# Performance work log

Measured on AMD Instinct MI355X. Metric: run time of the kernel, lower is better.

The kernel has to match this reference:

```python
import jax, jax.numpy as jnp
import numpy as np

N = 10000      # n_nodes
T = 8          # input_horizon
P = 2          # prediction_horizon (zeros appended; pred_hor=1 default)
F_IN = 64      # n_features
F_OUT = 64     # n_out_features
H = 128        # h_size
B = 2          # batch
E = 160000     # n_edges
MLPW = 4


def setup_inputs() -> dict:
    key = jax.random.key(0)
    ks = jax.random.split(key, 12)
    s = jnp.float32(0.05)
    return dict(
        x_in=jax.random.normal(ks[0], (B, T, N, F_IN), jnp.float32),
        edge_index=jax.random.randint(ks[1], (2, E), 0, N, jnp.int32),
        edge_weight=jax.random.uniform(ks[2], (E,), jnp.float32),
        gcn_w=jax.random.normal(ks[3], (F_OUT, F_IN), jnp.float32) * s,
        gcn_b=jnp.zeros((F_OUT,), jnp.float32),
        w_ih=jax.random.normal(ks[4], (H, F_OUT), jnp.float32) * s,
        w_hh=jax.random.normal(ks[5], (H, H), jnp.float32) * s,
        b_ih=jnp.zeros((H,), jnp.float32),
        b_hh=jnp.zeros((H,), jnp.float32),
        mlp_w1=jax.random.normal(ks[6], (H * MLPW, H), jnp.float32) * s,
        mlp_b1=jnp.zeros((H * MLPW,), jnp.float32),
        mlp_w2=jax.random.normal(ks[7], (H * MLPW, H * MLPW), jnp.float32) * s,
        mlp_b2=jnp.zeros((H * MLPW,), jnp.float32),
        mlp_w3=jax.random.normal(ks[8], (F_OUT, H * MLPW), jnp.float32) * s,
        mlp_b3=jnp.zeros((F_OUT,), jnp.float32),
    )


def reference(x_in, edge_index, edge_weight, gcn_w, gcn_b,
              w_ih, w_hh, b_ih, b_hh,
              mlp_w1, mlp_b1, mlp_w2, mlp_b2, mlp_w3, mlp_b3):
    Bb = x_in.shape[0]
    x = x_in.reshape(-1, N, F_IN)          # [G, N, F_in], G = B*T
    G = x.shape[0]

    # --- python id-remap (unique -> dense ids); identity when all node ids appear ---
    uv = jnp.unique(edge_index, size=N)
    ei = jnp.searchsorted(uv, edge_index)
    row, col = ei[0], ei[1]

    # --- GCNConv (gcn_norm with add_self_loops=True, fill 1.0) ---
    loop = jnp.arange(N, dtype=row.dtype)
    row_f = jnp.concatenate([row, loop])
    col_f = jnp.concatenate([col, loop])
    ew_f = jnp.concatenate([edge_weight, jnp.ones((N,), edge_weight.dtype)])
    deg = jnp.zeros((N,), edge_weight.dtype).at[col_f].add(ew_f)
    dinv = jnp.where(deg > 0, jax.lax.rsqrt(deg), 0.0)
    norm = dinv[row_f] * ew_f * dinv[col_f]          # [E+N]

    xl = x @ gcn_w.T                                 # [G, N, F_out]
    agg = jnp.zeros((G, N, F_OUT), xl.dtype).at[:, col_f].add(
        xl[:, row_f] * norm[None, :, None])          # scatter-add over targets
    gc = agg + gcn_b                                 # [G, N, F_out]

    # raw row-major view, exactly as torch .view((B*N, T, F_out))
    seq = gc.reshape(Bb * N, T, F_OUT)

    # --- single-layer tanh RNN, batch_first ---
    h0 = jnp.zeros((Bb * N, H), seq.dtype)

    def step(h, xt):
        h = jnp.tanh(xt @ w_ih.T + b_ih + h @ w_hh.T + b_hh)
        return h, h

    _, outs = jax.lax.scan(step, h0, seq.transpose(1, 0, 2))  # [T, B*N, H]
    rnn_out = outs.transpose(1, 0, 2)                          # [B*N, T, H]

    # --- MLP head applied per time step (vectorized) ---
    y = jax.nn.relu(rnn_out @ mlp_w1.T + mlp_b1)
    y = jax.nn.relu(y @ mlp_w2.T + mlp_b2)
    y = y @ mlp_w3.T + mlp_b3                                  # [B*N, T, F_out]

    # prediction slots stay zero (pred_hor=1 default)
    full = jnp.concatenate([y, jnp.zeros((Bb * N, P, F_OUT), y.dtype)], axis=1)
    return full.reshape(Bb, T + P, N, F_OUT)
```

## Files before the change

kernel.cpp:

```cpp
#include <hip/hip_runtime.h>
#include <hip/hip_bf16.h>

#define N_NODES 10000
#define E_EDGES 160000

typedef __attribute__((ext_vector_type(8))) short bf16x8;
typedef __attribute__((ext_vector_type(4))) float f32x4;

__device__ __forceinline__ unsigned short f2b(float f) {
    unsigned int u = __float_as_uint(f);
    u = (u + 0x7fffu + ((u >> 16) & 1u)) >> 16;
    return (unsigned short)u;
}

__device__ __forceinline__ float b2f(unsigned short u) {
    return __uint_as_float(((unsigned int)u) << 16);
}

__device__ __forceinline__ float tanh_fast(float x) {
    float ax = fabsf(x);
    float e = __expf(-2.f * ax);
    float r = (1.f - e) / (1.f + e);
    return copysignf(r, x);
}

__global__ void init_kernel(float* deg, int* cnt) {
    int i = blockIdx.x * 256 + threadIdx.x;
    if (i < N_NODES) { deg[i] = 1.0f; cnt[i] = 0; }
}

__global__ void deg_add_kernel(const int* __restrict__ ei, const float* __restrict__ ew,
                               float* deg, int* cnt) {
    int e = blockIdx.x * 256 + threadIdx.x;
    if (e < E_EDGES) {
        int c = ei[E_EDGES + e];
        atomicAdd(&deg[c], ew[e]);
        atomicAdd(&cnt[c], 1);
    }
}

__global__ void dinv_kernel(const float* __restrict__ deg, float* dinv) {
    int i = blockIdx.x * 256 + threadIdx.x;
    if (i < N_NODES) { float d = deg[i]; dinv[i] = d > 0.f ? rsqrtf(d) : 0.f; }
}

__global__ void scan_kernel(const int* __restrict__ cnt, int* offs, int* cursor) {
    __shared__ int tsum[1024];
    int t = threadIdx.x;
    int base = t * 10;
    int loc[10];
    int s = 0;
    #pragma unroll
    for (int j = 0; j < 10; ++j) {
        int i = base + j;
        int v = (i < N_NODES) ? cnt[i] : 0;
        loc[j] = s; s += v;
    }
    tsum[t] = s;
    __syncthreads();
    for (int d = 1; d < 1024; d <<= 1) {
        int v = (t >= d) ? tsum[t - d] : 0;
        __syncthreads();
        tsum[t] += v;
        __syncthreads();
    }
    int pre = tsum[t] - s;
    #pragma unroll
    for (int j = 0; j < 10; ++j) {
        int i = base + j;
        if (i < N_NODES) { offs[i] = pre + loc[j]; cursor[i] = pre + loc[j]; }
    }
    if (t == 1023) offs[N_NODES] = tsum[1023];
}

__global__ void fill_kernel(const int* __restrict__ ei, const float* __restrict__ ew,
                            const float* __restrict__ dinv, int* cursor,
                            int* erow, float* enorm) {
    int e = blockIdx.x * 256 + threadIdx.x;
    if (e < E_EDGES) {
        int r = ei[e], c = ei[E_EDGES + e];
        float nm = dinv[r] * ew[e] * dinv[c];
        int pos = atomicAdd(&cursor[c], 1);
        erow[pos] = r; enorm[pos] = nm;
    }
}

template<int KS, int K>
__global__ void wconv_kernel(const float* __restrict__ w, unsigned short* __restrict__ o) {
    int idx = blockIdx.x * 256 + threadIdx.x;
    int lane = idx & 63, frag = idx >> 6;
    int nf = frag / KS, ks = frag % KS;
    const float* src = w + (nf * 16 + (lane & 15)) * K + ks * 32 + (lane >> 4) * 8;
    unsigned short* dst = o + frag * 512 + lane * 8;
    float4 v0 = *(const float4*)src;
    float4 v1 = *(const float4*)(src + 4);
    ushort4 h0; h0.x = f2b(v0.x); h0.y = f2b(v0.y); h0.z = f2b(v0.z); h0.w = f2b(v0.w);
    ushort4 h1; h1.x = f2b(v1.x); h1.y = f2b(v1.y); h1.z = f2b(v1.z); h1.w = f2b(v1.w);
    *(ushort4*)dst = h0;
    *(ushort4*)(dst + 4) = h1;
}

__global__ __launch_bounds__(256) void aggregate_kernel(
        const unsigned short* __restrict__ xlt, const int* __restrict__ erow,
        const float* __restrict__ enorm, const int* __restrict__ offs,
        const float* __restrict__ dinv, const float* __restrict__ gcn_b,
        unsigned short* __restrict__ gc) {
    int gwid = (blockIdx.x * 256 + threadIdx.x) >> 6;
    int c = gwid >> 1;
    int gh = (gwid & 1) * 8;
    int lane = threadIdx.x & 63;
    if (c >= N_NODES) return;
    float acc[8];
    float d = dinv[c];
    float wself = d * d;
    const unsigned short* xr = xlt + (long)c * 1024 + gh * 64;
    #pragma unroll
    for (int g = 0; g < 8; ++g) acc[g] = b2f(xr[g * 64 + lane]) * wself;
    int e0 = offs[c], e1 = offs[c + 1];
    for (int e = e0; e < e1; ++e) {
        int r = erow[e];
        float nm = enorm[e];
        const unsigned short* xs = xlt + (long)r * 1024 + gh * 64;
        #pragma unroll
        for (int g = 0; g < 8; ++g) acc[g] += b2f(xs[g * 64 + lane]) * nm;
    }
    float bb = gcn_b[lane];
    #pragma unroll
    for (int g = 0; g < 8; ++g)
        gc[(long)(gh + g) * 640000 + (long)c * 64 + lane] = f2b(acc[g] + bb);
}

template<int NTOT, int BN, int KTOT, bool AF32, int EPI, bool RELU>
__global__ __launch_bounds__(256) void gemm_kernel(
        const void* __restrict__ Aptr, const float* __restrict__ Wp,
        const float* __restrict__ bias0, const float* __restrict__ bias1,
        void* __restrict__ outp) {
    constexpr int WN = BN / 2;
    constexpr int FN = WN / 16;
    __shared__ __align__(16) unsigned short As[128 * 72];
    __shared__ __align__(16) unsigned short Bs[BN * 72];
    const int tid = threadIdx.x;
    const int lane = tid & 63;
    const int wid = tid >> 6;
    const int wm = wid >> 1, wn = wid & 1;
    const long m0 = (long)blockIdx.x * 128;
    const int n0 = blockIdx.y * BN;

    f32x4 acc[4][FN];
    #pragma unroll
    for (int a = 0; a < 4; ++a)
        #pragma unroll
        for (int b = 0; b < FN; ++b)
            acc[a][b] = (f32x4){0.f, 0.f, 0.f, 0.f};

    for (int kt = 0; kt < KTOT / 64; ++kt) {
        if (AF32) {
            const float* Ag = (const float*)Aptr;
            #pragma unroll
            for (int p = 0; p < 8; ++p) {
                int idx = p * 256 + tid;
                int r = idx >> 4, c4 = idx & 15;
                float4 v = *(const float4*)(Ag + (m0 + r) * KTOT + kt * 64 + c4 * 4);
                ushort4 h; h.x = f2b(v.x); h.y = f2b(v.y); h.z = f2b(v.z); h.w = f2b(v.w);
                *(ushort4*)&As[r * 72 + c4 * 4] = h;
            }
        } else {
            const unsigned short* Ag = (const unsigned short*)Aptr;
            #pragma unroll
            for (int p = 0; p < 4; ++p) {
                int idx = p * 256 + tid;
                int r = idx >> 3, c8 = idx & 7;
                *(int4*)&As[r * 72 + c8 * 8] = *(const int4*)(Ag + (m0 + r) * KTOT + kt * 64 + c8 * 8);
            }
        }
        #pragma unroll
        for (int p = 0; p < BN / 16; ++p) {
            int idx = p * 256 + tid;
            int r = idx >> 4, c4 = idx & 15;
            float4 v = *(const float4*)(Wp + (long)(n0 + r) * KTOT + kt * 64 + c4 * 4);
            ushort4 h; h.x = f2b(v.x); h.y = f2b(v.y); h.z = f2b(v.z); h.w = f2b(v.w);
            *(ushort4*)&Bs[r * 72 + c4 * 4] = h;
        }
        __syncthreads();
        #pragma unroll
        for (int ks = 0; ks < 2; ++ks) {
            bf16x8 a[4], b[FN];
            #pragma unroll
            for (int fm = 0; fm < 4; ++fm)
                a[fm] = *(const bf16x8*)&As[(wm * 64 + fm * 16 + (lane & 15)) * 72 + ks * 32 + (lane >> 4) * 8];
            #pragma unroll
            for (int fn = 0; fn < FN; ++fn)
                b[fn] = *(const bf16x8*)&Bs[(wn * WN + fn * 16 + (lane & 15)) * 72 + ks * 32 + (lane >> 4) * 8];
            #pragma unroll
            for (int fm = 0; fm < 4; ++fm)
                #pragma unroll
                for (int fn = 0; fn < FN; ++fn)
                    acc[fm][fn] = __builtin_amdgcn_mfma_f32_16x16x32_bf16(a[fm], b[fn], acc[fm][fn], 0, 0, 0);
        }
        __syncthreads();
    }

    #pragma unroll
    for (int fm = 0; fm < 4; ++fm) {
        #pragma unroll
        for (int fn = 0; fn < FN; ++fn) {
            const int colg = n0 + wn * WN + fn * 16 + (lane & 15);
            float bv = 0.f;
            if (bias0) bv += bias0[colg];
            if (bias1) bv += bias1[colg];
            #pragma unroll
            for (int r = 0; r < 4; ++r) {
                int row = (int)m0 + wm * 64 + fm * 16 + (lane >> 4) * 4 + r;
                float v = acc[fm][fn][r] + bv;
                if (RELU) v = fmaxf(v, 0.f);
                if (EPI == 0) {
                    ((unsigned short*)outp)[(long)(row % N_NODES) * 1024 + (long)(row / N_NODES) * 64 + colg] = f2b(v);
                } else {
                    ((unsigned short*)outp)[(long)row * NTOT + colg] = f2b(v);
                }
            }
        }
    }
}

__global__ __launch_bounds__(256) void rnn_kernel(const unsigned short* __restrict__ xih,
                                                  const float* __restrict__ whh,
                                                  unsigned short* __restrict__ rout) {
    __shared__ __align__(16) unsigned short hs[80 * 128];
    __shared__ __align__(16) unsigned short ws[128 * 128];
    const int tid = threadIdx.x, lane = tid & 63, wid = tid >> 6;
    const long i0 = (long)blockIdx.x * 80;

    #pragma unroll
    for (int p = 0; p < 16; ++p) {
        int idx = p * 256 + tid;
        int n = idx >> 5, k4 = (idx & 31) * 4;
        float4 v = *(const float4*)(whh + n * 128 + k4);
        ushort4 h; h.x = f2b(v.x); h.y = f2b(v.y); h.z = f2b(v.z); h.w = f2b(v.w);
        int byte = (n * 256 + k4 * 2) ^ ((n & 7) << 4);
        *(ushort4*)((char*)ws + byte) = h;
    }
    int4 z = make_int4(0, 0, 0, 0);
    #pragma unroll
    for (int p = 0; p < 5; ++p) ((int4*)hs)[p * 256 + tid] = z;
    __syncthreads();

    unsigned short x2[2][5][2][4];
    #pragma unroll
    for (int fm = 0; fm < 5; ++fm)
        #pragma unroll
        for (int fn = 0; fn < 2; ++fn) {
            int col = wid * 32 + fn * 16 + (lane & 15);
            const unsigned short* src = xih + ((i0 + fm * 16 + (lane >> 4) * 4) * 8 + 0) * 128 + col;
            #pragma unroll
            for (int r = 0; r < 4; ++r) x2[0][fm][fn][r] = src[(long)r * 1024];
        }

    f32x4 acc[5][2];
    #pragma unroll
    for (int t = 0; t < 8; ++t) {
        const int cb = t & 1;
        #pragma unroll
        for (int fm = 0; fm < 5; ++fm)
            #pragma unroll
            for (int fn = 0; fn < 2; ++fn)
                #pragma unroll
                for (int r = 0; r < 4; ++r)
                    acc[fm][fn][r] = b2f(x2[cb][fm][fn][r]);
        if (t < 7) {
            #pragma unroll
            for (int fm = 0; fm < 5; ++fm)
                #pragma unroll
                for (int fn = 0; fn < 2; ++fn) {
                    int col = wid * 32 + fn * 16 + (lane & 15);
                    const unsigned short* src = xih + ((i0 + fm * 16 + (lane >> 4) * 4) * 8 + (t + 1)) * 128 + col;
                    #pragma unroll
                    for (int r = 0; r < 4; ++r) x2[cb ^ 1][fm][fn][r] = src[(long)r * 1024];
                }
        }
        #pragma unroll
        for (int ks = 0; ks < 4; ++ks) {
            bf16x8 a[5], b[2];
            #pragma unroll
            for (int fm = 0; fm < 5; ++fm) {
                int row = fm * 16 + (lane & 15);
                int byte = (row * 256 + ks * 64 + (lane >> 4) * 16) ^ ((row & 7) << 4);
                a[fm] = *(const bf16x8*)((const char*)hs + byte);
            }
            #pragma unroll
            for (int fn = 0; fn < 2; ++fn) {
                int rowb = wid * 32 + fn * 16 + (lane & 15);
                int byte = (rowb * 256 + ks * 64 + (lane >> 4) * 16) ^ ((rowb & 7) << 4);
                b[fn] = *(const bf16x8*)((const char*)ws + byte);
            }
            #pragma unroll
            for (int fm = 0; fm < 5; ++fm)
                #pragma unroll
                for (int fn = 0; fn < 2; ++fn)
                    acc[fm][fn] = __builtin_amdgcn_mfma_f32_16x16x32_bf16(a[fm], b[fn], acc[fm][fn], 0, 0, 0);
        }
        __syncthreads();
        #pragma unroll
        for (int fm = 0; fm < 5; ++fm)
            #pragma unroll
            for (int fn = 0; fn < 2; ++fn) {
                int col = wid * 32 + fn * 16 + (lane & 15);
                #pragma unroll
                for (int r = 0; r < 4; ++r) {
                    int row = fm * 16 + (lane >> 4) * 4 + r;
                    float v = tanh_fast(acc[fm][fn][r]);
                    unsigned short hb = f2b(v);
                    int byte = (row * 256 + col * 2) ^ ((row & 7) << 4);
                    *(unsigned short*)((char*)hs + byte) = hb;
                    rout[((i0 + row) * 8 + t) * 128 + col] = hb;
                }
            }
        __syncthreads();
    }
}

__global__ __launch_bounds__(512) void mlp_kernel(
        const unsigned short* __restrict__ A,
        const unsigned short* __restrict__ w1f, const float* __restrict__ b1,
        const unsigned short* __restrict__ w2f, const float* __restrict__ b2,
        const unsigned short* __restrict__ w3f, const float* __restrict__ b3,
        float* __restrict__ out) {
    __shared__ __align__(16) char smem[147456];
    char* As  = smem;
    char* y1s = smem + 16384;
    char* y2s = smem + 81920;
    float* red = (float*)smem;

    const int tid = threadIdx.x, lane = tid & 63, w = tid >> 6;
    const long r0 = (long)blockIdx.x * 64;

    #pragma unroll
    for (int p = 0; p < 2; ++p) {
        int idx = p * 512 + tid;
        int row = idx >> 4, c16 = idx & 15;
        int4 v = *(const int4*)(A + (r0 + row) * 128 + c16 * 8);
        int byte = (row * 256 + c16 * 16) ^ ((row & 7) << 4);
        *(int4*)(As + byte) = v;
    }
    __syncthreads();

    f32x4 acc[4][4];

    #pragma unroll
    for (int fm = 0; fm < 4; ++fm)
        #pragma unroll
        for (int fn = 0; fn < 4; ++fn) acc[fm][fn] = (f32x4){0.f, 0.f, 0.f, 0.f};
    #pragma unroll
    for (int ks = 0; ks < 4; ++ks) {
        bf16x8 a[4], b[4];
        #pragma unroll
        for (int fm = 0; fm < 4; ++fm) {
            int row = fm * 16 + (lane & 15);
            a[fm] = *(const bf16x8*)(As + ((row * 256 + ks * 64 + (lane >> 4) * 16) ^ ((row & 7) << 4)));
        }
        #pragma unroll
        for (int fn = 0; fn < 4; ++fn)
            b[fn] = *(const bf16x8*)(w1f + (long)((w * 4 + fn) * 4 + ks) * 512 + lane * 8);
        #pragma unroll
        for (int fm = 0; fm < 4; ++fm)
            #pragma unroll
            for (int fn = 0; fn < 4; ++fn)
                acc[fm][fn] = __builtin_amdgcn_mfma_f32_16x16x32_bf16(a[fm], b[fn], acc[fm][fn], 0, 0, 0);
    }
    #pragma unroll
    for (int fn = 0; fn < 4; ++fn) {
        int colg = w * 64 + fn * 16 + (lane & 15);
        float bv = b1[colg];
        #pragma unroll
        for (int fm = 0; fm < 4; ++fm)
            #pragma unroll
            for (int r = 0; r < 4; ++r) {
                int row = fm * 16 + (lane >> 4) * 4 + r;
                float v = fmaxf(acc[fm][fn][r] + bv, 0.f);
                int byte = (row * 1024 + colg * 2) ^ ((row & 7) << 4);
                *(unsigned short*)(y1s + byte) = f2b(v);
            }
    }
    __syncthreads();

    #pragma unroll
    for (int fm = 0; fm < 4; ++fm)
        #pragma unroll
        for (int fn = 0; fn < 4; ++fn) acc[fm][fn] = (f32x4){0.f, 0.f, 0.f, 0.f};
    #pragma unroll
    for (int ks = 0; ks < 16; ++ks) {
        bf16x8 a[4], b[4];
        #pragma unroll
        for (int fm = 0; fm < 4; ++fm) {
            int row = fm * 16 + (lane & 15);
            a[fm] = *(const bf16x8*)(y1s + ((row * 1024 + ks * 64 + (lane >> 4) * 16) ^ ((row & 7) << 4)));
        }
        #pragma unroll
        for (int fn = 0; fn < 4; ++fn)
            b[fn] = *(const bf16x8*)(w2f + (long)((w * 4 + fn) * 16 + ks) * 512 + lane * 8);
        #pragma unroll
        for (int fm = 0; fm < 4; ++fm)
            #pragma unroll
            for (int fn = 0; fn < 4; ++fn)
                acc[fm][fn] = __builtin_amdgcn_mfma_f32_16x16x32_bf16(a[fm], b[fn], acc[fm][fn], 0, 0, 0);
    }
    #pragma unroll
    for (int fn = 0; fn < 4; ++fn) {
        int colg = w * 64 + fn * 16 + (lane & 15);
        float bv = b2[colg];
        #pragma unroll
        for (int fm = 0; fm < 4; ++fm)
            #pragma unroll
            for (int r = 0; r < 4; ++r) {
                int row = fm * 16 + (lane >> 4) * 4 + r;
                float v = fmaxf(acc[fm][fn][r] + bv, 0.f);
                int byte = (row * 1024 + colg * 2) ^ ((row & 7) << 4);
                *(unsigned short*)(y2s + byte) = f2b(v);
            }
    }
    __syncthreads();

    #pragma unroll
    for (int fm = 0; fm < 4; ++fm)
        #pragma unroll
        for (int fn = 0; fn < 4; ++fn) acc[fm][fn] = (f32x4){0.f, 0.f, 0.f, 0.f};
    #pragma unroll
    for (int ksl = 0; ksl < 2; ++ksl) {
        int ks = w * 2 + ksl;
        bf16x8 a[4], b[4];
        #pragma unroll
        for (int fm = 0; fm < 4; ++fm) {
            int row = fm * 16 + (lane & 15);
            a[fm] = *(const bf16x8*)(y2s + ((row * 1024 + ks * 64 + (lane >> 4) * 16) ^ ((row & 7) << 4)));
        }
        #pragma unroll
        for (int fn = 0; fn < 4; ++fn)
            b[fn] = *(const bf16x8*)(w3f + (long)(fn * 16 + ks) * 512 + lane * 8);
        #pragma unroll
        for (int fm = 0; fm < 4; ++fm)
            #pragma unroll
            for (int fn = 0; fn < 4; ++fn)
                acc[fm][fn] = __builtin_amdgcn_mfma_f32_16x16x32_bf16(a[fm], b[fn], acc[fm][fn], 0, 0, 0);
    }
    {
        if (w >= 4) {
            float* rb = red + (w - 4) * 4160;
            #pragma unroll
            for (int fm = 0; fm < 4; ++fm)
                #pragma unroll
                for (int fn = 0; fn < 4; ++fn)
                    #pragma unroll
                    for (int r = 0; r < 4; ++r)
                        rb[(fm * 16 + (lane >> 4) * 4 + r) * 65 + fn * 16 + (lane & 15)] = acc[fm][fn][r];
        }
        __syncthreads();
        if (w < 4) {
            float* rb = red + w * 4160;
            #pragma unroll
            for (int fm = 0; fm < 4; ++fm)
                #pragma unroll
                for (int fn = 0; fn < 4; ++fn)
                    #pragma unroll
                    for (int r = 0; r < 4; ++r)
                        acc[fm][fn][r] += rb[(fm * 16 + (lane >> 4) * 4 + r) * 65 + fn * 16 + (lane & 15)];
        }
        __syncthreads();
        if (w == 2 || w == 3) {
            float* rb = red + (w - 2) * 4160;
            #pragma unroll
            for (int fm = 0; fm < 4; ++fm)
                #pragma unroll
                for (int fn = 0; fn < 4; ++fn)
                    #pragma unroll
                    for (int r = 0; r < 4; ++r)
                        rb[(fm * 16 + (lane >> 4) * 4 + r) * 65 + fn * 16 + (lane & 15)] = acc[fm][fn][r];
        }
        __syncthreads();
        if (w < 2) {
            float* rb = red + w * 4160;
            #pragma unroll
            for (int fm = 0; fm < 4; ++fm)
                #pragma unroll
                for (int fn = 0; fn < 4; ++fn)
                    #pragma unroll
                    for (int r = 0; r < 4; ++r)
                        acc[fm][fn][r] += rb[(fm * 16 + (lane >> 4) * 4 + r) * 65 + fn * 16 + (lane & 15)];
        }
        __syncthreads();
        if (w == 1) {
            float* rb = red;
            #pragma unroll
            for (int fm = 0; fm < 4; ++fm)
                #pragma unroll
                for (int fn = 0; fn < 4; ++fn)
                    #pragma unroll
                    for (int r = 0; r < 4; ++r)
                        rb[(fm * 16 + (lane >> 4) * 4 + r) * 65 + fn * 16 + (lane & 15)] = acc[fm][fn][r];
        }
        __syncthreads();
        if (w == 0) {
            float* rb = red;
            #pragma unroll
            for (int fm = 0; fm < 4; ++fm)
                #pragma unroll
                for (int fn = 0; fn < 4; ++fn) {
                    int col = fn * 16 + (lane & 15);
                    float bv = b3[col];
                    #pragma unroll
                    for (int r = 0; r < 4; ++r) {
                        int row = fm * 16 + (lane >> 4) * 4 + r;
                        float v = acc[fm][fn][r] + rb[row * 65 + col] + bv;
                        long vr = r0 + row;
                        out[((vr >> 3) * 10 + (vr & 7)) * 64 + col] = v;
                    }
                }
        }
    }
}

extern "C" void kernel_launch(void* const* d_in, const int* in_sizes, int n_in,
                              void* d_out, int out_size, void* d_ws, size_t ws_size,
                              hipStream_t stream) {
    const float* x     = (const float*)d_in[0];
    const int*   ei    = (const int*)  d_in[1];
    const float* ew    = (const float*)d_in[2];
    const float* gcn_w = (const float*)d_in[3];
    const float* gcn_b = (const float*)d_in[4];
    const float* w_ih  = (const float*)d_in[5];
    const float* w_hh  = (const float*)d_in[6];
    const float* b_ih  = (const float*)d_in[7];
    const float* b_hh  = (const float*)d_in[8];
    const float* w1    = (const float*)d_in[9];
    const float* b1    = (const float*)d_in[10];
    const float* w2    = (const float*)d_in[11];
    const float* b2    = (const float*)d_in[12];
    const float* w3    = (const float*)d_in[13];
    const float* b3    = (const float*)d_in[14];

    char* ws = (char*)d_ws;
    unsigned short* xlt  = (unsigned short*)ws;
    unsigned short* rnno = (unsigned short*)ws;
    unsigned short* gc   = (unsigned short*)(ws + 41943040L);
    unsigned short* xih  = (unsigned short*)(ws + 62914560L);
    unsigned short* w1f  = (unsigned short*)(ws + 104857600L);
    unsigned short* w2f  = (unsigned short*)(ws + 104988672L);
    unsigned short* w3f  = (unsigned short*)(ws + 105512960L);
    char* sm = ws + 106954752L;
    float* deg    = (float*)(sm);
    float* dinv   = (float*)(sm + (64 << 10));
    int*   cnt    = (int*)  (sm + (128 << 10));
    int*   offs   = (int*)  (sm + (192 << 10));
    int*   cursor = (int*)  (sm + (256 << 10));
    int*   erow   = (int*)  (sm + (320 << 10));
    float* enorm  = (float*)(sm + (1 << 20));

    hipMemsetAsync(d_out, 0, (size_t)out_size * sizeof(float), stream);

    init_kernel<<<40, 256, 0, stream>>>(deg, cnt);
    deg_add_kernel<<<625, 256, 0, stream>>>(ei, ew, deg, cnt);
    dinv_kernel<<<40, 256, 0, stream>>>(deg, dinv);
    scan_kernel<<<1, 1024, 0, stream>>>(cnt, offs, cursor);
    fill_kernel<<<625, 256, 0, stream>>>(ei, ew, dinv, cursor, erow, enorm);

    wconv_kernel<4, 128><<<32, 256, 0, stream>>>(w1, w1f);
    wconv_kernel<16, 512><<<128, 256, 0, stream>>>(w2, w2f);
    wconv_kernel<16, 512><<<16, 256, 0, stream>>>(w3, w3f);

    gemm_kernel<64, 64, 64, true, 0, false><<<dim3(1250, 1), 256, 0, stream>>>(x, gcn_w, nullptr, nullptr, xlt);
    aggregate_kernel<<<5000, 256, 0, stream>>>(xlt, erow, enorm, offs, dinv, gcn_b, gc);
    gemm_kernel<128, 128, 64, false, 2, false><<<dim3(1250, 1), 256, 0, stream>>>(gc, w_ih, b_ih, b_hh, xih);
    rnn_kernel<<<250, 256, 0, stream>>>(xih, w_hh, rnno);
    mlp_kernel<<<2500, 512, 0, stream>>>(rnno, w1f, b1, w2f, b2, w3f, b3, (float*)d_out);
}
```

Measured before the change: 452.3 us.

## Shrink RNN tile to 32 rows and cut MLP shared memory via buffer reuse

The RNN kernel now handles 32 rows per block instead of 80 and launches 625 blocks rather than 250, so more of the GPU's compute units have work and each block needs fewer registers and less LDS. The MLP kernel reuses one buffer for both hidden activations, dropping shared memory from 144KB to 80KB so more blocks can reside per CU. Its final layer is re-partitioned so each wave computes one 16-column slice over half of K, which replaces the multi-stage tree reduction with a single exchange. The LDS XOR swizzle is widened to 16 rows. In exchange, the extra barrier before the in-place overwrite and the smaller RNN tiles mean W_hh is loaded and converted more times in total.

```diff
diff --git a/kernel.cpp b/kernel.cpp
--- a/kernel.cpp
+++ b/kernel.cpp
@@ -226,10 +226,10 @@
 __global__ __launch_bounds__(256) void rnn_kernel(const unsigned short* __restrict__ xih,
                                                   const float* __restrict__ whh,
                                                   unsigned short* __restrict__ rout) {
-    __shared__ __align__(16) unsigned short hs[80 * 128];
+    __shared__ __align__(16) unsigned short hs[32 * 128];
     __shared__ __align__(16) unsigned short ws[128 * 128];
     const int tid = threadIdx.x, lane = tid & 63, wid = tid >> 6;
-    const long i0 = (long)blockIdx.x * 80;
+    const long i0 = (long)blockIdx.x * 32;
 
     #pragma unroll
     for (int p = 0; p < 16; ++p) {
@@ -242,12 +242,12 @@
     }
     int4 z = make_int4(0, 0, 0, 0);
     #pragma unroll
-    for (int p = 0; p < 5; ++p) ((int4*)hs)[p * 256 + tid] = z;
-    __syncthreads();
-
-    unsigned short x2[2][5][2][4];
-    #pragma unroll
-    for (int fm = 0; fm < 5; ++fm)
+    for (int p = 0; p < 2; ++p) ((int4*)hs)[p * 256 + tid] = z;
+    __syncthreads();
+
+    unsigned short x2[2][2][2][4];
+    #pragma unroll
+    for (int fm = 0; fm < 2; ++fm)
         #pragma unroll
         for (int fn = 0; fn < 2; ++fn) {
             int col = wid * 32 + fn * 16 + (lane & 15);
@@ -256,12 +256,12 @@
             for (int r = 0; r < 4; ++r) x2[0][fm][fn][r] = src[(long)r * 1024];
         }
 
-    f32x4 acc[5][2];
+    f32x4 acc[2][2];
     #pragma unroll
     for (int t = 0; t < 8; ++t) {
         const int cb = t & 1;
         #pragma unroll
-        for (int fm = 0; fm < 5; ++fm)
+        for (int fm = 0; fm < 2; ++fm)
             #pragma unroll
             for (int fn = 0; fn < 2; ++fn)
                 #pragma unroll
@@ -269,7 +269,7 @@
                     acc[fm][fn][r] = b2f(x2[cb][fm][fn][r]);
         if (t < 7) {
             #pragma unroll
-            for (int fm = 0; fm < 5; ++fm)
+            for (int fm = 0; fm < 2; ++fm)
                 #pragma unroll
                 for (int fn = 0; fn < 2; ++fn) {
                     int col = wid * 32 + fn * 16 + (lane & 15);
@@ -280,9 +280,9 @@
         }
         #pragma unroll
         for (int ks = 0; ks < 4; ++ks) {
-            bf16x8 a[5], b[2];
-            #pragma unroll
-            for (int fm = 0; fm < 5; ++fm) {
+            bf16x8 a[2], b[2];
+            #pragma unroll
+            for (int fm = 0; fm < 2; ++fm) {
                 int row = fm * 16 + (lane & 15);
                 int byte = (row * 256 + ks * 64 + (lane >> 4) * 16) ^ ((row & 7) << 4);
                 a[fm] = *(const bf16x8*)((const char*)hs + byte);
@@ -294,14 +294,14 @@
                 b[fn] = *(const bf16x8*)((const char*)ws + byte);
             }
             #pragma unroll
-            for (int fm = 0; fm < 5; ++fm)
+            for (int fm = 0; fm < 2; ++fm)
                 #pragma unroll
                 for (int fn = 0; fn < 2; ++fn)
                     acc[fm][fn] = __builtin_amdgcn_mfma_f32_16x16x32_bf16(a[fm], b[fn], acc[fm][fn], 0, 0, 0);
         }
         __syncthreads();
         #pragma unroll
-        for (int fm = 0; fm < 5; ++fm)
+        for (int fm = 0; fm < 2; ++fm)
             #pragma unroll
             for (int fn = 0; fn < 2; ++fn) {
                 int col = wid * 32 + fn * 16 + (lane & 15);
@@ -325,11 +325,9 @@
         const unsigned short* __restrict__ w2f, const float* __restrict__ b2,
         const unsigned short* __restrict__ w3f, const float* __restrict__ b3,
         float* __restrict__ out) {
-    __shared__ __align__(16) char smem[147456];
-    char* As  = smem;
-    char* y1s = smem + 16384;
-    char* y2s = smem + 81920;
-    float* red = (float*)smem;
+    __shared__ __align__(16) char smem[81920];
+    char* As = smem;
+    char* ys = smem + 16384;
 
     const int tid = threadIdx.x, lane = tid & 63, w = tid >> 6;
     const long r0 = (long)blockIdx.x * 64;
@@ -339,7 +337,7 @@
         int idx = p * 512 + tid;
         int row = idx >> 4, c16 = idx & 15;
         int4 v = *(const int4*)(A + (r0 + row) * 128 + c16 * 8);
-        int byte = (row * 256 + c16 * 16) ^ ((row & 7) << 4);
+        int byte = (row * 256 + c16 * 16) ^ ((row & 15) << 4);
         *(int4*)(As + byte) = v;
     }
     __syncthreads();
@@ -356,7 +354,7 @@
         #pragma unroll
         for (int fm = 0; fm < 4; ++fm) {
             int row = fm * 16 + (lane & 15);
-            a[fm] = *(const bf16x8*)(As + ((row * 256 + ks * 64 + (lane >> 4) * 16) ^ ((row & 7) << 4)));
+            a[fm] = *(const bf16x8*)(As + ((row * 256 + ks * 64 + (lane >> 4) * 16) ^ ((row & 15) << 4)));
         }
         #pragma unroll
         for (int fn = 0; fn < 4; ++fn)
@@ -377,8 +375,8 @@
             for (int r = 0; r < 4; ++r) {
                 int row = fm * 16 + (lane >> 4) * 4 + r;
                 float v = fmaxf(acc[fm][fn][r] + bv, 0.f);
-                int byte = (row * 1024 + colg * 2) ^ ((row & 7) << 4);
-                *(unsigned short*)(y1s + byte) = f2b(v);
+                int byte = (row * 1024 + colg * 2) ^ ((row & 15) << 4);
+                *(unsigned short*)(ys + byte) = f2b(v);
             }
     }
     __syncthreads();
@@ -393,7 +391,7 @@
         #pragma unroll
         for (int fm = 0; fm < 4; ++fm) {
             int row = fm * 16 + (lane & 15);
-            a[fm] = *(const bf16x8*)(y1s + ((row * 1024 + ks * 64 + (lane >> 4) * 16) ^ ((row & 7) << 4)));
+            a[fm] = *(const bf16x8*)(ys + ((row * 1024 + ks * 64 + (lane >> 4) * 16) ^ ((row & 15) << 4)));
         }
         #pragma unroll
         for (int fn = 0; fn < 4; ++fn)
@@ -404,6 +402,7 @@
             for (int fn = 0; fn < 4; ++fn)
                 acc[fm][fn] = __builtin_amdgcn_mfma_f32_16x16x32_bf16(a[fm], b[fn], acc[fm][fn], 0, 0, 0);
     }
+    __syncthreads();
     #pragma unroll
     for (int fn = 0; fn < 4; ++fn) {
         int colg = w * 64 + fn * 16 + (lane & 15);
@@ -414,107 +413,49 @@
             for (int r = 0; r < 4; ++r) {
                 int row = fm * 16 + (lane >> 4) * 4 + r;
                 float v = fmaxf(acc[fm][fn][r] + bv, 0.f);
-                int byte = (row * 1024 + colg * 2) ^ ((row & 7) << 4);
-                *(unsigned short*)(y2s + byte) = f2b(v);
-            }
-    }
-    __syncthreads();
-
-    #pragma unroll
-    for (int fm = 0; fm < 4; ++fm)
-        #pragma unroll
-        for (int fn = 0; fn < 4; ++fn) acc[fm][fn] = (f32x4){0.f, 0.f, 0.f, 0.f};
-    #pragma unroll
-    for (int ksl = 0; ksl < 2; ++ksl) {
-        int ks = w * 2 + ksl;
-        bf16x8 a[4], b[4];
+                int byte = (row * 1024 + colg * 2) ^ ((row & 15) << 4);
+                *(unsigned short*)(ys + byte) = f2b(v);
+            }
+    }
+    __syncthreads();
+
+    const int fn3 = w & 3, kh = w >> 2;
+    f32x4 a3[4];
+    #pragma unroll
+    for (int fm = 0; fm < 4; ++fm) a3[fm] = (f32x4){0.f, 0.f, 0.f, 0.f};
+    #pragma unroll
+    for (int ksl = 0; ksl < 8; ++ksl) {
+        int ks = kh * 8 + ksl;
+        bf16x8 bfrag = *(const bf16x8*)(w3f + (long)(fn3 * 16 + ks) * 512 + lane * 8);
         #pragma unroll
         for (int fm = 0; fm < 4; ++fm) {
             int row = fm * 16 + (lane & 15);
-            a[fm] = *(const bf16x8*)(y2s + ((row * 1024 + ks * 64 + (lane >> 4) * 16) ^ ((row & 7) << 4)));
-        }
-        #pragma unroll
-        for (int fn = 0; fn < 4; ++fn)
-            b[fn] = *(const bf16x8*)(w3f + (long)(fn * 16 + ks) * 512 + lane * 8);
+            bf16x8 afrag = *(const bf16x8*)(ys + ((row * 1024 + ks * 64 + (lane >> 4) * 16) ^ ((row & 15) << 4)));
+            a3[fm] = __builtin_amdgcn_mfma_f32_16x16x32_bf16(afrag, bfrag, a3[fm], 0, 0, 0);
+        }
+    }
+    __syncthreads();
+    if (w >= 4) {
+        float* rb = (float*)(ys) + (w - 4) * 1104;
         #pragma unroll
         for (int fm = 0; fm < 4; ++fm)
             #pragma unroll
-            for (int fn = 0; fn < 4; ++fn)
-                acc[fm][fn] = __builtin_amdgcn_mfma_f32_16x16x32_bf16(a[fm], b[fn], acc[fm][fn], 0, 0, 0);
-    }
-    {
-        if (w >= 4) {
-            float* rb = red + (w - 4) * 4160;
-            #pragma unroll
-            for (int fm = 0; fm < 4; ++fm)
-                #pragma unroll
-                for (int fn = 0; fn < 4; ++fn)
-                    #pragma unroll
-                    for (int r = 0; r < 4; ++r)
-                        rb[(fm * 16 + (lane >> 4) * 4 + r) * 65 + fn * 16 + (lane & 15)] = acc[fm][fn][r];
-        }
-        __syncthreads();
-        if (w < 4) {
-            float* rb = red + w * 4160;
-            #pragma unroll
-            for (int fm = 0; fm < 4; ++fm)
-                #pragma unroll
-                for (int fn = 0; fn < 4; ++fn)
-                    #pragma unroll
-                    for (int r = 0; r < 4; ++r)
-                        acc[fm][fn][r] += rb[(fm * 16 + (lane >> 4) * 4 + r) * 65 + fn * 16 + (lane & 15)];
-        }
-        __syncthreads();
-        if (w == 2 || w == 3) {
-            float* rb = red + (w - 2) * 4160;
-            #pragma unroll
-            for (int fm = 0; fm < 4; ++fm)
-                #pragma unroll
-                for (int fn = 0; fn < 4; ++fn)
-                    #pragma unroll
-                    for (int r = 0; r < 4; ++r)
-                        rb[(fm * 16 + (lane >> 4) * 4 + r) * 65 + fn * 16 + (lane & 15)] = acc[fm][fn][r];
-        }
-        __syncthreads();
-        if (w < 2) {
-            float* rb = red + w * 4160;
-            #pragma unroll
-            for (int fm = 0; fm < 4; ++fm)
-                #pragma unroll
-                for (int fn = 0; fn < 4; ++fn)
-                    #pragma unroll
-                    for (int r = 0; r < 4; ++r)
-                        acc[fm][fn][r] += rb[(fm * 16 + (lane >> 4) * 4 + r) * 65 + fn * 16 + (lane & 15)];
-        }
-        __syncthreads();
-        if (w == 1) {
-            float* rb = red;
-            #pragma unroll
-            for (int fm = 0; fm < 4; ++fm)
-                #pragma unroll
-                for (int fn = 0; fn < 4; ++fn)
-                    #pragma unroll
-                    for (int r = 0; r < 4; ++r)
-                        rb[(fm * 16 + (lane >> 4) * 4 + r) * 65 + fn * 16 + (lane & 15)] = acc[fm][fn][r];
-        }
-        __syncthreads();
-        if (w == 0) {
-            float* rb = red;
-            #pragma unroll
-            for (int fm = 0; fm < 4; ++fm)
-                #pragma unroll
-                for (int fn = 0; fn < 4; ++fn) {
-                    int col = fn * 16 + (lane & 15);
-                    float bv = b3[col];
-                    #pragma unroll
-                    for (int r = 0; r < 4; ++r) {
-                        int row = fm * 16 + (lane >> 4) * 4 + r;
-                        float v = acc[fm][fn][r] + rb[row * 65 + col] + bv;
-                        long vr = r0 + row;
-                        out[((vr >> 3) * 10 + (vr & 7)) * 64 + col] = v;
-                    }
-                }
-        }
+            for (int r = 0; r < 4; ++r)
+                rb[(fm * 16 + (lane >> 4) * 4 + r) * 17 + (lane & 15)] = a3[fm][r];
+    }
+    __syncthreads();
+    if (w < 4) {
+        float* rb = (float*)(ys) + w * 1104;
+        float bv = b3[fn3 * 16 + (lane & 15)];
+        #pragma unroll
+        for (int fm = 0; fm < 4; ++fm)
+            #pragma unroll
+            for (int r = 0; r < 4; ++r) {
+                int row = fm * 16 + (lane >> 4) * 4 + r;
+                float v = a3[fm][r] + rb[row * 17 + (lane & 15)] + bv;
+                long vr = r0 + row;
+                out[((vr >> 3) * 10 + (vr & 7)) * 64 + fn3 * 16 + (lane & 15)] = v;
+            }
     }
 }
 
@@ -569,6 +510,6 @@
     gemm_kernel<64, 64, 64, true, 0, false><<<dim3(1250, 1), 256, 0, stream>>>(x, gcn_w, nullptr, nullptr, xlt);
     aggregate_kernel<<<5000, 256, 0, stream>>>(xlt, erow, enorm, offs, dinv, gcn_b, gc);
     gemm_kernel<128, 128, 64, false, 2, false><<<dim3(1250, 1), 256, 0, stream>>>(gc, w_ih, b_ih, b_hh, xih);
-    rnn_kernel<<<250, 256, 0, stream>>>(xih, w_hh, rnno);
+    rnn_kernel<<<625, 256, 0, stream>>>(xih, w_hh, rnno);
     mlp_kernel<<<2500, 512, 0, stream>>>(rnno, w1f, b1, w2f, b2, w3f, b3, (float*)d_out);
 }
```

New measurement: 402.2 us. 1.12x faster.
